# Kernel tuning notes

Measured on AMD Instinct MI355X. Metric: run time of the kernel, lower is better.

Reference implementation:

```python
import jax, jax.numpy as jnp
import numpy as np

N = 16777216
NC = 262144

def setup_inputs() -> dict:
    key = jax.random.key(0)
    k1, k2 = jax.random.split(key)
    site_energy = jax.random.normal(k1, (N, 1), dtype=jnp.float32)
    segment_ids = jnp.sort(jax.random.randint(k2, (N,), 0, NC, dtype=jnp.int64))
    return {"site_energy": site_energy, "segment_ids": segment_ids, "num_crystals": NC}

def reference(site_energy, segment_ids, num_crystals):
    flat = site_energy.squeeze(-1)                                   # [N]
    total = jax.ops.segment_sum(flat, segment_ids, num_segments=num_crystals)
    counts = jax.ops.segment_sum(jnp.ones_like(flat), segment_ids, num_segments=num_crystals)
    return (total / jnp.maximum(counts, 1.0))[:, None]               # [nc,1]
```

## Files before the change

kernel.cpp:

```cpp
#include <hip/hip_runtime.h>
#include <hip/hip_bf16.h>


#define VPT 16

__global__ void seg_sum_kernel(const float* __restrict__ x,
                               const void* __restrict__ seg,
                               float* __restrict__ sums,
                               float* __restrict__ cnts,
                               int n) {
    const int* s32 = (const int*)seg;
    const long long* s64 = (const long long*)seg;
    const bool is64 = (s32[n - 1] == 0);

    const long long base = (long long)(blockIdx.x * (long long)blockDim.x + threadIdx.x) * VPT;
    const int lane = threadIdx.x & 63;

    int ids[VPT];
    float vals[VPT];
    int nv = 0;
    if (base < n) {
        long long rem = (long long)n - base;
        nv = (rem >= VPT) ? VPT : (int)rem;
    }

    if (nv == VPT) {
        const float4* xv = (const float4*)(x + base);
        #pragma unroll
        for (int k = 0; k < 4; ++k) {
            float4 a = xv[k];
            vals[4 * k]     = a.x;
            vals[4 * k + 1] = a.y;
            vals[4 * k + 2] = a.z;
            vals[4 * k + 3] = a.w;
        }
        if (is64) {
            const int4* iv = (const int4*)(s64 + base);
            #pragma unroll
            for (int k = 0; k < 8; ++k) {
                int4 t = iv[k];
                ids[2 * k]     = t.x;
                ids[2 * k + 1] = t.z;
            }
        } else {
            const int4* iv = (const int4*)(s32 + base);
            #pragma unroll
            for (int k = 0; k < 4; ++k) {
                int4 t = iv[k];
                ids[4 * k]     = t.x;
                ids[4 * k + 1] = t.y;
                ids[4 * k + 2] = t.z;
                ids[4 * k + 3] = t.w;
            }
        }
    } else {
        #pragma unroll
        for (int k = 0; k < VPT; ++k) {
            if (k < nv) {
                ids[k]  = is64 ? (int)s64[base + k] : s32[base + k];
                vals[k] = x[base + k];
            } else {
                ids[k]  = -1;
                vals[k] = 0.0f;
            }
        }
    }

    int   cur = (nv > 0) ? ids[0] : -1;
    float s   = (nv > 0) ? vals[0] : 0.0f;
    float c   = (nv > 0) ? 1.0f : 0.0f;
    #pragma unroll
    for (int k = 1; k < VPT; ++k) {
        if (k < nv) {
            if (ids[k] == cur) {
                s += vals[k];
                c += 1.0f;
            } else {
                atomicAdd(&sums[cur], s);
                atomicAdd(&cnts[cur], c);
                cur = ids[k];
                s = vals[k];
                c = 1.0f;
            }
        }
    }

    int lid = cur;
    #pragma unroll
    for (int off = 1; off < 64; off <<= 1) {
        float os = __shfl_up(s, off);
        float oc = __shfl_up(c, off);
        int  oid = __shfl_up(lid, off);
        if (lane >= off && oid == lid) {
            s += os;
            c += oc;
        }
    }

    int nid = __shfl_down(lid, 1);
    bool emit = (lid >= 0) && ((lane == 63) || (nid != lid));
    if (emit) {
        atomicAdd(&sums[lid], s);
        atomicAdd(&cnts[lid], c);
    }
}

__global__ void finalize_kernel(float* __restrict__ out,
                                const float* __restrict__ sums,
                                const float* __restrict__ cnts,
                                int nc) {
    int cidx = blockIdx.x * blockDim.x + threadIdx.x;
    if (cidx < nc) {
        out[cidx] = sums[cidx] / fmaxf(cnts[cidx], 1.0f);
    }
}

extern "C" void kernel_launch(void* const* d_in, const int* in_sizes, int n_in,
                              void* d_out, int out_size, void* d_ws, size_t ws_size,
                              hipStream_t stream) {
    const float* x = (const float*)d_in[0];
    const void* seg = d_in[1];
    const int n = in_sizes[0];
    const int nc = out_size;

    float* sums = (float*)d_ws;
    float* cnts = (float*)d_ws + nc;
    float* out  = (float*)d_out;

    hipMemsetAsync(sums, 0, (size_t)2 * nc * sizeof(float), stream);

    const int block = 256;
    const long long elems_per_block = (long long)block * VPT;
    const int grid = (int)((n + elems_per_block - 1) / elems_per_block);
    seg_sum_kernel<<<grid, block, 0, stream>>>(x, seg, sums, cnts, n);

    const int fgrid = (nc + block - 1) / block;
    finalize_kernel<<<fgrid, block, 0, stream>>>(out, sums, cnts, nc);
}
```

Measured before the change: 41.20 us.

## Accumulate segments in shared memory per block and write interior means directly

Replaces the wavefront shuffle-scan plus global atomics with per-block shared-memory atomic accumulation, indexed by segment id relative to the block's first id. Segments lying entirely inside a block have their mean written straight to the output. Only boundary segments go through global atomics and the finalize pass, which now writes only segments that have a count. This cuts global atomic traffic, but adds an extra memset of the output, two block barriers, and 32KB of LDS per block, which may reduce occupancy.

```diff
diff --git a/kernel.cpp b/kernel.cpp
--- a/kernel.cpp
+++ b/kernel.cpp
@@ -3,18 +3,27 @@
 
 
 #define VPT 16
+#define BLOCK 256
+#define CHUNK (VPT * BLOCK)
 
-__global__ void seg_sum_kernel(const float* __restrict__ x,
-                               const void* __restrict__ seg,
-                               float* __restrict__ sums,
-                               float* __restrict__ cnts,
-                               int n) {
+__global__ __launch_bounds__(BLOCK)
+void seg_mean_kernel(const float* __restrict__ x,
+                     const void* __restrict__ seg,
+                     float* __restrict__ out,
+                     float* __restrict__ gsums,
+                     float* __restrict__ gcnts,
+                     int n) {
+    __shared__ float lsum[CHUNK];
+    __shared__ float lcnt[CHUNK];
+    __shared__ int s_first, s_last;
+
     const int* s32 = (const int*)seg;
     const long long* s64 = (const long long*)seg;
     const bool is64 = (s32[n - 1] == 0);
 
-    const long long base = (long long)(blockIdx.x * (long long)blockDim.x + threadIdx.x) * VPT;
-    const int lane = threadIdx.x & 63;
+    const int tid = threadIdx.x;
+    const long long bbase = (long long)blockIdx.x * CHUNK;
+    const long long base = bbase + (long long)tid * VPT;
 
     int ids[VPT];
     float vals[VPT];
@@ -66,52 +75,93 @@
         }
     }
 
-    int   cur = (nv > 0) ? ids[0] : -1;
-    float s   = (nv > 0) ? vals[0] : 0.0f;
-    float c   = (nv > 0) ? 1.0f : 0.0f;
-    #pragma unroll
-    for (int k = 1; k < VPT; ++k) {
-        if (k < nv) {
-            if (ids[k] == cur) {
-                s += vals[k];
-                c += 1.0f;
-            } else {
-                atomicAdd(&sums[cur], s);
-                atomicAdd(&cnts[cur], c);
-                cur = ids[k];
-                s = vals[k];
-                c = 1.0f;
+    if (tid == 0) s_first = ids[0];
+    {
+        long long lastpos = bbase + CHUNK;
+        if (lastpos > n) lastpos = n;
+        lastpos -= 1;
+        int lt = (int)((lastpos - bbase) / VPT);
+        int le = (int)((lastpos - bbase) % VPT);
+        if (tid == lt) s_last = ids[le];
+    }
+
+    {
+        float4 z = make_float4(0.f, 0.f, 0.f, 0.f);
+        float4* ls4 = (float4*)lsum;
+        float4* lc4 = (float4*)lcnt;
+        #pragma unroll
+        for (int k = tid; k < CHUNK / 4; k += BLOCK) {
+            ls4[k] = z;
+            lc4[k] = z;
+        }
+    }
+    __syncthreads();
+
+    const int first = s_first;
+
+    if (nv > 0) {
+        int   cur = ids[0];
+        float s   = vals[0];
+        float c   = 1.0f;
+        #pragma unroll
+        for (int k = 1; k < VPT; ++k) {
+            if (k < nv) {
+                if (ids[k] == cur) {
+                    s += vals[k];
+                    c += 1.0f;
+                } else {
+                    int off = cur - first;
+                    if (off < CHUNK) {
+                        atomicAdd(&lsum[off], s);
+                        atomicAdd(&lcnt[off], c);
+                    } else {
+                        atomicAdd(&gsums[cur], s);
+                        atomicAdd(&gcnts[cur], c);
+                    }
+                    cur = ids[k];
+                    s = vals[k];
+                    c = 1.0f;
+                }
             }
         }
-    }
-
-    int lid = cur;
-    #pragma unroll
-    for (int off = 1; off < 64; off <<= 1) {
-        float os = __shfl_up(s, off);
-        float oc = __shfl_up(c, off);
-        int  oid = __shfl_up(lid, off);
-        if (lane >= off && oid == lid) {
-            s += os;
-            c += oc;
+        int off = cur - first;
+        if (off < CHUNK) {
+            atomicAdd(&lsum[off], s);
+            atomicAdd(&lcnt[off], c);
+        } else {
+            atomicAdd(&gsums[cur], s);
+            atomicAdd(&gcnts[cur], c);
         }
     }
+    __syncthreads();
 
-    int nid = __shfl_down(lid, 1);
-    bool emit = (lid >= 0) && ((lane == 63) || (nid != lid));
-    if (emit) {
-        atomicAdd(&sums[lid], s);
-        atomicAdd(&cnts[lid], c);
+    int span = s_last - first + 1;
+    int lim = (span < CHUNK) ? span : CHUNK;
+    for (int idx = tid; idx < lim; idx += BLOCK) {
+        float sv = lsum[idx];
+        float cv = lcnt[idx];
+        int gc = first + idx;
+        if (idx == 0 || idx == lim - 1) {
+            if (cv > 0.0f) {
+                atomicAdd(&gsums[gc], sv);
+                atomicAdd(&gcnts[gc], cv);
+            }
+        } else {
+            out[gc] = (cv > 0.0f) ? (sv / cv) : 0.0f;
+        }
     }
 }
 
 __global__ void finalize_kernel(float* __restrict__ out,
-                                const float* __restrict__ sums,
-                                const float* __restrict__ cnts,
+                                const float* __restrict__ gsums,
+                                const float* __restrict__ gcnts,
                                 int nc) {
-    int cidx = blockIdx.x * blockDim.x + threadIdx.x;
-    if (cidx < nc) {
-        out[cidx] = sums[cidx] / fmaxf(cnts[cidx], 1.0f);
+    int c = blockIdx.x * blockDim.x + threadIdx.x;
+    if (c < nc) {
+        float cv = gcnts[c];
+        if (cv > 0.0f) {
+            out[c] = gsums[c] / cv;
+        }
     }
 }
 
@@ -123,17 +173,16 @@
     const int n = in_sizes[0];
     const int nc = out_size;
 
-    float* sums = (float*)d_ws;
-    float* cnts = (float*)d_ws + nc;
-    float* out  = (float*)d_out;
+    float* gsums = (float*)d_ws;
+    float* gcnts = (float*)d_ws + nc;
+    float* out   = (float*)d_out;
 
-    hipMemsetAsync(sums, 0, (size_t)2 * nc * sizeof(float), stream);
+    hipMemsetAsync(out, 0, (size_t)nc * sizeof(float), stream);
+    hipMemsetAsync(gsums, 0, (size_t)2 * nc * sizeof(float), stream);
 
-    const int block = 256;
-    const long long elems_per_block = (long long)block * VPT;
-    const int grid = (int)((n + elems_per_block - 1) / elems_per_block);
-    seg_sum_kernel<<<grid, block, 0, stream>>>(x, seg, sums, cnts, n);
+    const int grid = (int)(((long long)n + CHUNK - 1) / CHUNK);
+    seg_mean_kernel<<<grid, BLOCK, 0, stream>>>(x, seg, out, gsums, gcnts, n);
 
-    const int fgrid = (nc + block - 1) / block;
-    finalize_kernel<<<fgrid, block, 0, stream>>>(out, sums, cnts, nc);
+    const int fgrid = (nc + BLOCK - 1) / BLOCK;
+    finalize_kernel<<<fgrid, BLOCK, 0, stream>>>(out, gsums, gcnts, nc);
 }
```

After: 42.65 us. +3.5%, slower.
